# Performance work log

Measured on AMD Instinct MI355X. Metric: run time of the kernel, lower is better.

## Reference

```python
import jax, jax.numpy as jnp
import numpy as np

D_MODEL = 1024
NUM_HEADS = 16
D_K = D_MODEL // NUM_HEADS


def setup_inputs() -> dict:
    key = jax.random.key(0)
    ks = jax.random.split(key, 11)
    B, S = 4, 2048
    s = 1.0 / np.sqrt(D_MODEL)
    inp = {
        "q": jax.random.normal(ks[0], (B, S, D_MODEL), jnp.float32),
        "k": jax.random.normal(ks[1], (B, S, D_MODEL), jnp.float32),
        "v": jax.random.normal(ks[2], (B, S, D_MODEL), jnp.float32),
        "w_q": jax.random.normal(ks[3], (D_MODEL, D_MODEL), jnp.float32) * s,
        "b_q": jnp.zeros((D_MODEL,), jnp.float32),
        "w_k": jax.random.normal(ks[4], (D_MODEL, D_MODEL), jnp.float32) * s,
        "b_k": jnp.zeros((D_MODEL,), jnp.float32),
        "w_v": jax.random.normal(ks[5], (D_MODEL, D_MODEL), jnp.float32) * s,
        "b_v": jnp.zeros((D_MODEL,), jnp.float32),
        "w_o": jax.random.normal(ks[6], (D_MODEL, D_MODEL), jnp.float32) * s,
        "b_o": jnp.zeros((D_MODEL,), jnp.float32),
    }
    return inp


def reference(q, k, v, w_q, b_q, w_k, b_k, w_v, b_v, w_o, b_o):
    B, S, _ = q.shape
    # projections; weights stored as [in, out] so x @ W + b
    def proj(x, w, b):
        y = x @ w + b  # [B, S, d_model]
        return y.reshape(B, -1, NUM_HEADS, D_K).transpose(0, 2, 1, 3)  # [B,H,S,d_k]
    qh = proj(q, w_q, b_q)
    kh = proj(k, w_k, b_k)
    vh = proj(v, w_v, b_v)
    scores = jnp.einsum("bhsd,bhtd->bhst", qh, kh) / jnp.sqrt(jnp.float32(D_K))
    attn = jax.nn.softmax(scores, axis=-1)  # dropout p=0.0 -> identity
    x = jnp.einsum("bhst,bhtd->bhsd", attn, vh)
    x = x.transpose(0, 2, 1, 3).reshape(B, S, D_MODEL)
    return x @ w_o + b_o
```

## Files before the change

### kernel.cpp

```cpp
#include <hip/hip_runtime.h>
#include <hip/hip_bf16.h>
#include <stdint.h>

#define D_MODEL 1024
#define SEQ 2048
#define BATCH 4
#define NHEADS 16
#define ROWS (BATCH*SEQ)

#define QKSCALE 0.18033688011f

typedef __attribute__((ext_vector_type(4))) float f32x4;
typedef __attribute__((ext_vector_type(8))) short short8;
typedef __attribute__((ext_vector_type(4))) unsigned int uint4v;

#if __has_builtin(__builtin_amdgcn_exp2f)
#define EXP2(x) __builtin_amdgcn_exp2f(x)
#else
#define EXP2(x) exp2f(x)
#endif

__device__ __forceinline__ unsigned short f2bf(float f) {
    unsigned int x = __builtin_bit_cast(unsigned int, f);
    x += 0x7fffu + ((x >> 16) & 1u);
    return (unsigned short)(x >> 16);
}

__device__ __forceinline__ unsigned int cvtpk(float a, float b) {
    unsigned int r;
    asm("v_cvt_pk_bf16_f32 %0, %1, %2" : "=v"(r) : "v"(a), "v"(b));
    return r;
}

__device__ __forceinline__ void gload16(const unsigned short* src, unsigned short* dst) {
    __builtin_amdgcn_global_load_lds(
        (const __attribute__((address_space(1))) void*)src,
        (__attribute__((address_space(3))) void*)dst, 16, 0, 0);
}

__global__ __launch_bounds__(256) void wtrans_kernel(const float* __restrict__ w0,
                                                     const float* __restrict__ w1,
                                                     const float* __restrict__ w2,
                                                     const float* __restrict__ w3,
                                                     unsigned short* __restrict__ wt0,
                                                     unsigned short* __restrict__ wt1,
                                                     unsigned short* __restrict__ wt2,
                                                     unsigned short* __restrict__ wt3) {
    const int z = blockIdx.z;
    const float* w = (z == 0) ? w0 : (z == 1) ? w1 : (z == 2) ? w2 : w3;
    unsigned short* wt = (z == 0) ? wt0 : (z == 1) ? wt1 : (z == 2) ? wt2 : wt3;
    __shared__ float tile[32][33];
    int tx = threadIdx.x & 31;
    int ty = threadIdx.x >> 5;
    int r0 = blockIdx.y * 32, c0 = blockIdx.x * 32;
    #pragma unroll
    for (int i = 0; i < 4; ++i)
        tile[ty + 8*i][tx] = w[(size_t)(r0 + ty + 8*i) * D_MODEL + (c0 + tx)];
    __syncthreads();
    int t = threadIdx.x;
    if (t < 128) {
        int n_loc = t >> 2;
        int kc = t & 3;
        int n = c0 + n_loc;
        int kbase = r0 + kc*8;
        uint4v pk;
        #pragma unroll
        for (int j = 0; j < 4; ++j)
            pk[j] = cvtpk(tile[kc*8 + 2*j][n_loc], tile[kc*8 + 2*j + 1][n_loc]);
        size_t tidx = (size_t)(n >> 7) * 16 + (kbase >> 6);
        int row = n & 127;
        int byte = (row*128 + (kbase & 63)*2) ^ ((row & 7) << 4);
        *(uint4v*)((char*)wt + tidx*16384 + byte) = pk;
    }
}

__global__ __launch_bounds__(256) void qkv_gemm_kernel(
        const float* __restrict__ qin, const float* __restrict__ kin,
        const float* __restrict__ vin,
        const unsigned short* __restrict__ wqt, const unsigned short* __restrict__ wkt,
        const unsigned short* __restrict__ wvt,
        const float* __restrict__ bq, const float* __restrict__ bk,
        const float* __restrict__ bv,
        unsigned short* __restrict__ qhd, unsigned short* __restrict__ khd,
        unsigned short* __restrict__ vtd) {
    __shared__ __attribute__((aligned(16))) unsigned short Alds[128*64];
    __shared__ __attribute__((aligned(16))) unsigned short Blds[2][128*64];
    const int z = blockIdx.z;
    const float* Af = (z == 0) ? qin : (z == 1) ? kin : vin;
    const unsigned short* Bt = (z == 0) ? wqt : (z == 1) ? wkt : wvt;
    const float* bias = (z == 0) ? bq : (z == 1) ? bk : bv;
    const int m0 = blockIdx.x * 128;
    const int n0 = blockIdx.y * 128;
    const int t = threadIdx.x;
    const int lane = t & 63;
    const int w = t >> 6;
    const int wm = w >> 1, wn = w & 1;
    const int l15 = lane & 15, lg = lane >> 4;
    const unsigned short* tbase = Bt + (size_t)(n0 >> 7) * 16 * 8192;

    f32x4 acc[4][4];
    #pragma unroll
    for (int i = 0; i < 4; ++i)
        #pragma unroll
        for (int j = 0; j < 4; ++j) acc[i][j] = (f32x4)(0.0f);

    #pragma unroll
    for (int i = 0; i < 8; ++i) {
        int idx = t + i*256;
        int row = idx >> 4, c4 = idx & 15;
        f32x4 v = *(const f32x4*)(Af + (size_t)(m0+row)*D_MODEL + c4*4);
        unsigned long long pk = (unsigned long long)cvtpk(v[0], v[1])
                              | ((unsigned long long)cvtpk(v[2], v[3]) << 32);
        int byte = (row*128 + c4*8) ^ ((row & 7) << 4);
        *(unsigned long long*)((char*)Alds + byte) = pk;
    }
    #pragma unroll
    for (int i = 0; i < 4; ++i)
        gload16(tbase + t*8 + i*2048, Blds[0] + t*8 + i*2048);
    __syncthreads();

    #pragma unroll 2
    for (int kt = 0; kt < 16; ++kt) {
        const int cur = kt & 1, nxt = cur ^ 1;
        f32x4 av[8];
        if (kt < 15) {
            const int k0n = (kt + 1) * 64;
            #pragma unroll
            for (int i = 0; i < 8; ++i) {
                int idx = t + i*256;
                int row = idx >> 4, c4 = idx & 15;
                av[i] = *(const f32x4*)(Af + (size_t)(m0+row)*D_MODEL + k0n + c4*4);
            }
            const unsigned short* tsrc = tbase + (size_t)(kt + 1) * 8192;
            #pragma unroll
            for (int i = 0; i < 4; ++i)
                gload16(tsrc + t*8 + i*2048, Blds[nxt] + t*8 + i*2048);
        }

        #pragma unroll
        for (int kk = 0; kk < 2; ++kk) {
            short8 af[4], bfr[4];
            #pragma unroll
            for (int mi = 0; mi < 4; ++mi) {
                int row = wm*64 + mi*16 + l15;
                int byte = (row*128 + kk*64 + lg*16) ^ ((row & 7) << 4);
                af[mi] = *(const short8*)((const char*)Alds + byte);
            }
            #pragma unroll
            for (int ni = 0; ni < 4; ++ni) {
                int row = wn*64 + ni*16 + l15;
                int byte = (row*128 + kk*64 + lg*16) ^ ((row & 7) << 4);
                bfr[ni] = *(const short8*)((const char*)Blds[cur] + byte);
            }
            #pragma unroll
            for (int mi = 0; mi < 4; ++mi)
                #pragma unroll
                for (int ni = 0; ni < 4; ++ni)
                    acc[mi][ni] = __builtin_amdgcn_mfma_f32_16x16x32_bf16(
                        af[mi], bfr[ni], acc[mi][ni], 0, 0, 0);
        }
        __syncthreads();
        if (kt < 15) {
            #pragma unroll
            for (int i = 0; i < 8; ++i) {
                int idx = t + i*256;
                int row = idx >> 4, c4 = idx & 15;
                unsigned long long pk = (unsigned long long)cvtpk(av[i][0], av[i][1])
                                      | ((unsigned long long)cvtpk(av[i][2], av[i][3]) << 32);
                int byte = (row*128 + c4*8) ^ ((row & 7) << 4);
                *(unsigned long long*)((char*)Alds + byte) = pk;
            }
            __syncthreads();
        }
    }

    #pragma unroll
    for (int mi = 0; mi < 4; ++mi)
        #pragma unroll
        for (int ni = 0; ni < 4; ++ni) {
            int col = n0 + wn*64 + ni*16 + l15;
            float bv_ = bias[col];
            int h = col >> 6, d = col & 63;
            if (z == 0) {
                #pragma unroll
                for (int r = 0; r < 4; ++r) {
                    int row = m0 + wm*64 + mi*16 + lg*4 + r;
                    int bb = row >> 11, s = row & 2047;
                    float vv = (acc[mi][ni][r] + bv_) * QKSCALE;
                    qhd[(((size_t)(bb*NHEADS + h)*SEQ + s) << 6) + d] = f2bf(vv);
                }
            } else if (z == 1) {
                #pragma unroll
                for (int r = 0; r < 4; ++r) {
                    int row = m0 + wm*64 + mi*16 + lg*4 + r;
                    int bb = row >> 11, s = row & 2047;
                    int ti = s >> 6, kvl = s & 63;
                    int ph = (kvl & 0x23) | ((kvl & 4) << 2) | ((kvl & 0x18) >> 1);
                    int byte = (ph*128 + d*2) ^ ((ph & 7) << 4);
                    *(unsigned short*)((char*)khd
                        + ((size_t)(bb*NHEADS + h)*32 + ti)*8192 + byte)
                        = f2bf(acc[mi][ni][r] + bv_);
                }
            } else {
                int row0 = m0 + wm*64 + mi*16 + lg*4;
                int bb = row0 >> 11, s0 = row0 & 2047;
                int ti = s0 >> 6, kvl0 = s0 & 63;
                unsigned long long pk = 0;
                #pragma unroll
                for (int r = 0; r < 4; ++r)
                    pk |= (unsigned long long)f2bf(acc[mi][ni][r] + bv_) << (16*r);
                int byte = (d*128 + kvl0*2) ^ ((d & 7) << 4);
                *(unsigned long long*)((char*)vtd
                    + ((size_t)(bb*NHEADS + h)*32 + ti)*8192 + byte) = pk;
            }
        }
}

__global__ __launch_bounds__(256) void out_gemm_kernel(const unsigned short* __restrict__ Ab,
                                                       const unsigned short* __restrict__ Bt,
                                                       const float* __restrict__ bias,
                                                       float* __restrict__ Out) {
    __shared__ __attribute__((aligned(16))) unsigned short Alds[128*64];
    __shared__ __attribute__((aligned(16))) unsigned short Blds[2][128*64];
    const int m0 = blockIdx.x * 128;
    const int n0 = blockIdx.y * 128;
    const int t = threadIdx.x;
    const int lane = t & 63;
    const int w = t >> 6;
    const int wm = w >> 1, wn = w & 1;
    const int l15 = lane & 15, lg = lane >> 4;
    const unsigned short* tbase = Bt + (size_t)(n0 >> 7) * 16 * 8192;

    f32x4 acc[4][4];
    #pragma unroll
    for (int i = 0; i < 4; ++i)
        #pragma unroll
        for (int j = 0; j < 4; ++j) acc[i][j] = (f32x4)(0.0f);

    #pragma unroll
    for (int i = 0; i < 4; ++i) {
        int idx = t + i*256;
        int row = idx >> 3, c8 = idx & 7;
        short8 v = *(const short8*)(Ab + (size_t)(m0+row)*D_MODEL + c8*8);
        int byte = (row*128 + c8*16) ^ ((row & 7) << 4);
        *(short8*)((char*)Alds + byte) = v;
    }
    #pragma unroll
    for (int i = 0; i < 4; ++i)
        gload16(tbase + t*8 + i*2048, Blds[0] + t*8 + i*2048);
    __syncthreads();

    #pragma unroll 2
    for (int kt = 0; kt < 16; ++kt) {
        const int cur = kt & 1, nxt = cur ^ 1;
        short8 av8[4];
        if (kt < 15) {
            const int k0n = (kt + 1) * 64;
            #pragma unroll
            for (int i = 0; i < 4; ++i) {
                int idx = t + i*256;
                int row = idx >> 3, c8 = idx & 7;
                av8[i] = *(const short8*)(Ab + (size_t)(m0+row)*D_MODEL + k0n + c8*8);
            }
            const unsigned short* tsrc = tbase + (size_t)(kt + 1) * 8192;
            #pragma unroll
            for (int i = 0; i < 4; ++i)
                gload16(tsrc + t*8 + i*2048, Blds[nxt] + t*8 + i*2048);
        }

        #pragma unroll
        for (int kk = 0; kk < 2; ++kk) {
            short8 af[4], bfr[4];
            #pragma unroll
            for (int mi = 0; mi < 4; ++mi) {
                int row = wm*64 + mi*16 + l15;
                int byte = (row*128 + kk*64 + lg*16) ^ ((row & 7) << 4);
                af[mi] = *(const short8*)((const char*)Alds + byte);
            }
            #pragma unroll
            for (int ni = 0; ni < 4; ++ni) {
                int row = wn*64 + ni*16 + l15;
                int byte = (row*128 + kk*64 + lg*16) ^ ((row & 7) << 4);
                bfr[ni] = *(const short8*)((const char*)Blds[cur] + byte);
            }
            #pragma unroll
            for (int mi = 0; mi < 4; ++mi)
                #pragma unroll
                for (int ni = 0; ni < 4; ++ni)
                    acc[mi][ni] = __builtin_amdgcn_mfma_f32_16x16x32_bf16(
                        af[mi], bfr[ni], acc[mi][ni], 0, 0, 0);
        }
        __syncthreads();
        if (kt < 15) {
            #pragma unroll
            for (int i = 0; i < 4; ++i) {
                int idx = t + i*256;
                int row = idx >> 3, c8 = idx & 7;
                int byte = (row*128 + c8*16) ^ ((row & 7) << 4);
                *(short8*)((char*)Alds + byte) = av8[i];
            }
            __syncthreads();
        }
    }

    #pragma unroll
    for (int mi = 0; mi < 4; ++mi)
        #pragma unroll
        for (int ni = 0; ni < 4; ++ni) {
            int col = n0 + wn*64 + ni*16 + l15;
            float bv_ = bias[col];
            #pragma unroll
            for (int r = 0; r < 4; ++r) {
                int row = m0 + wm*64 + mi*16 + lg*4 + r;
                Out[(size_t)row*D_MODEL + col] = acc[mi][ni][r] + bv_;
            }
        }
}

__global__ __launch_bounds__(256, 4) void attn_kernel(const unsigned short* __restrict__ qh,
                                                      const unsigned short* __restrict__ kimg_all,
                                                      const unsigned short* __restrict__ vimg_all,
                                                      unsigned short* __restrict__ xout) {
    __shared__ __attribute__((aligned(16))) unsigned short Klds[2][64*64];
    __shared__ __attribute__((aligned(16))) unsigned short Vtl[2][64*64];

    const int bid = blockIdx.x;
    const int xcd = bid & 7, idx = bid >> 3;
    const int qb = idx >> 3;
    const int bh = ((idx & 7) << 3) | xcd;
    const int t = threadIdx.x;
    const int lane = t & 63;
    const int w = t >> 6;
    const int l15 = lane & 15, lg = lane >> 4;

    const unsigned short* qbase = qh + (size_t)bh * SEQ * 64;
    const unsigned short* kimg = kimg_all + (size_t)bh * SEQ * 64;
    const unsigned short* vimg = vimg_all + (size_t)bh * SEQ * 64;

    short8 qf[2][2];
    #pragma unroll
    for (int l = 0; l < 2; ++l) {
        int qrow = qb*128 + w*32 + l*16 + l15;
        qf[l][0] = *(const short8*)(qbase + (size_t)qrow*64 + lg*8);
        qf[l][1] = *(const short8*)(qbase + (size_t)qrow*64 + 32 + lg*8);
    }

    int fb[4][2];
    #pragma unroll
    for (int nb = 0; nb < 4; ++nb) {
        int rr = nb*16 + l15;
        int sw = (rr & 7) << 4;
        fb[nb][0] = (rr*128 + lg*16) ^ sw;
        fb[nb][1] = (rr*128 + 64 + lg*16) ^ sw;
    }

    float m[2] = {-1e30f, -1e30f};
    float lsum[2] = {0.f, 0.f};
    f32x4 o[2][4];
    #pragma unroll
    for (int l = 0; l < 2; ++l)
        #pragma unroll
        for (int nb = 0; nb < 4; ++nb) o[l][nb] = (f32x4)(0.0f);

    #pragma unroll
    for (int i = 0; i < 2; ++i) {
        __builtin_amdgcn_global_load_lds(
            (const __attribute__((address_space(1))) void*)(kimg + t*8 + i*2048),
            (__attribute__((address_space(3))) void*)(Klds[0] + t*8 + i*2048), 16, 0, 0);
        __builtin_amdgcn_global_load_lds(
            (const __attribute__((address_space(1))) void*)(vimg + t*8 + i*2048),
            (__attribute__((address_space(3))) void*)(Vtl[0] + t*8 + i*2048), 16, 0, 0);
    }
    __syncthreads();

    const unsigned short* kp = kimg + 4096 + t*8;
    const unsigned short* vp = vimg + 4096 + t*8;

    const int NT = SEQ/64;
    #pragma unroll 2
    for (int ti = 0; ti < NT; ++ti) {
        const int c = ti & 1;
        if (ti + 1 < NT) {
            #pragma unroll
            for (int i = 0; i < 2; ++i) {
                __builtin_amdgcn_global_load_lds(
                    (const __attribute__((address_space(1))) void*)(kp + i*2048),
                    (__attribute__((address_space(3))) void*)(Klds[c^1] + t*8 + i*2048), 16, 0, 0);
                __builtin_amdgcn_global_load_lds(
                    (const __attribute__((address_space(1))) void*)(vp + i*2048),
                    (__attribute__((address_space(3))) void*)(Vtl[c^1] + t*8 + i*2048), 16, 0, 0);
            }
            kp += 4096; vp += 4096;
        }
        const char* Kc = (const char*)Klds[c];
        const char* Vc = (const char*)Vtl[c];

        f32x4 s4[2][4];
        #pragma unroll
        for (int nb = 0; nb < 4; ++nb) {
            short8 kf0 = *(const short8*)(Kc + fb[nb][0]);
            short8 kf1 = *(const short8*)(Kc + fb[nb][1]);
            __builtin_amdgcn_s_setprio(1);
            #pragma unroll
            for (int l = 0; l < 2; ++l) {
                f32x4 s = (f32x4)(0.0f);
                s = __builtin_amdgcn_mfma_f32_16x16x32_bf16(kf0, qf[l][0], s, 0, 0, 0);
                s = __builtin_amdgcn_mfma_f32_16x16x32_bf16(kf1, qf[l][1], s, 0, 0, 0);
                s4[l][nb] = s;
            }
            __builtin_amdgcn_s_setprio(0);
        }

        if (ti == 0) {
            #pragma unroll
            for (int l = 0; l < 2; ++l) {
                float tm = s4[l][0][0];
                #pragma unroll
                for (int nb = 0; nb < 4; ++nb)
                    #pragma unroll
                    for (int r = 0; r < 4; ++r) tm = fmaxf(tm, s4[l][nb][r]);
                tm = fmaxf(tm, __shfl_xor(tm, 16));
                tm = fmaxf(tm, __shfl_xor(tm, 32));
                m[l] = tm;
            }
        }

        union U { short8 s; unsigned int u[4]; } pa[2][2];
        #pragma unroll
        for (int l = 0; l < 2; ++l) {
            float p[16];
            float ts = 0.f;
            #pragma unroll
            for (int nb = 0; nb < 4; ++nb)
                #pragma unroll
                for (int r = 0; r < 4; ++r) {
                    float pv = EXP2(s4[l][nb][r] - m[l]);
                    p[nb*4 + r] = pv;
                    ts += pv;
                }
            lsum[l] += ts;

            pa[l][0].u[0] = cvtpk(p[0],  p[1]);  pa[l][0].u[1] = cvtpk(p[2],  p[3]);
            pa[l][0].u[2] = cvtpk(p[4],  p[5]);  pa[l][0].u[3] = cvtpk(p[6],  p[7]);
            pa[l][1].u[0] = cvtpk(p[8],  p[9]);  pa[l][1].u[1] = cvtpk(p[10], p[11]);
            pa[l][1].u[2] = cvtpk(p[12], p[13]); pa[l][1].u[3] = cvtpk(p[14], p[15]);
        }

        #pragma unroll
        for (int nb = 0; nb < 4; ++nb) {
            short8 vf0 = *(const short8*)(Vc + fb[nb][0]);
            short8 vf1 = *(const short8*)(Vc + fb[nb][1]);
            __builtin_amdgcn_s_setprio(1);
            o[0][nb] = __builtin_amdgcn_mfma_f32_16x16x32_bf16(pa[0][0].s, vf0, o[0][nb], 0, 0, 0);
            o[0][nb] = __builtin_amdgcn_mfma_f32_16x16x32_bf16(pa[0][1].s, vf1, o[0][nb], 0, 0, 0);
            o[1][nb] = __builtin_amdgcn_mfma_f32_16x16x32_bf16(pa[1][0].s, vf0, o[1][nb], 0, 0, 0);
            o[1][nb] = __builtin_amdgcn_mfma_f32_16x16x32_bf16(pa[1][1].s, vf1, o[1][nb], 0, 0, 0);
            __builtin_amdgcn_s_setprio(0);
        }

        __syncthreads();
    }

    const int bb = bh >> 4, h = bh & 15;
    #pragma unroll
    for (int l = 0; l < 2; ++l) {
        float lt = lsum[l];
        lt += __shfl_xor(lt, 16);
        lt += __shfl_xor(lt, 32);
        float rl[4];
        #pragma unroll
        for (int r = 0; r < 4; ++r) rl[r] = 1.0f / __shfl(lt, lg*4 + r);
        #pragma unroll
        for (int nb = 0; nb < 4; ++nb)
            #pragma unroll
            for (int r = 0; r < 4; ++r) {
                int s = qb*128 + w*32 + l*16 + lg*4 + r;
                int d = nb*16 + l15;
                xout[((size_t)(bb*SEQ + s))*D_MODEL + h*64 + d] = f2bf(o[l][nb][r] * rl[r]);
            }
    }
}

extern "C" void kernel_launch(void* const* d_in, const int* in_sizes, int n_in,
                              void* d_out, int out_size, void* d_ws, size_t ws_size,
                              hipStream_t stream) {
    (void)in_sizes; (void)n_in; (void)out_size; (void)ws_size;
    const float* q  = (const float*)d_in[0];
    const float* k  = (const float*)d_in[1];
    const float* v  = (const float*)d_in[2];
    const float* wq = (const float*)d_in[3];
    const float* bq = (const float*)d_in[4];
    const float* wk = (const float*)d_in[5];
    const float* bk = (const float*)d_in[6];
    const float* wv = (const float*)d_in[7];
    const float* bv = (const float*)d_in[8];
    const float* wo = (const float*)d_in[9];
    const float* bo = (const float*)d_in[10];

    char* ws = (char*)d_ws;
    unsigned short* wqt = (unsigned short*)(ws);
    unsigned short* wkt = (unsigned short*)(ws + (2ull << 20));
    unsigned short* wvt = (unsigned short*)(ws + (4ull << 20));
    unsigned short* wot = (unsigned short*)(ws + (6ull << 20));
    unsigned short* qhd = (unsigned short*)(ws + (8ull << 20));
    unsigned short* khd = (unsigned short*)(ws + (24ull << 20));
    unsigned short* vtd = (unsigned short*)(ws + (40ull << 20));
    unsigned short* xat = (unsigned short*)(ws + (56ull << 20));

    hipLaunchKernelGGL(wtrans_kernel, dim3(D_MODEL/32, D_MODEL/32, 4), dim3(256), 0, stream,
                       wq, wk, wv, wo, wqt, wkt, wvt, wot);

    hipLaunchKernelGGL(qkv_gemm_kernel, dim3(ROWS/128, D_MODEL/128, 3), dim3(256), 0, stream,
                       q, k, v, wqt, wkt, wvt, bq, bk, bv, qhd, khd, vtd);

    hipLaunchKernelGGL(attn_kernel, dim3(16*64), dim3(256), 0, stream,
                       qhd, khd, vtd, xat);

    hipLaunchKernelGGL(out_gemm_kernel, dim3(ROWS/128, D_MODEL/128), dim3(256), 0, stream,
                       xat, wot, bo, (float*)d_out);
}
```

Baseline: 189.4 us.

## Software-pipeline attention loop: overlap QK^T of next tile with PV of previous

Restructures the attention inner loop so each iteration computes QK^T for tile ti while doing the PV matmul for tile ti-1 with already-packed probabilities, then runs softmax on the new scores. V is triple-buffered in LDS to keep the previous tile alive while prefetching. The aim is to hide exp/softmax latency behind MFMA work. It adds a prologue and epilogue and uses more LDS, which may reduce occupancy. The loop is also no longer unrolled.

```diff
diff --git a/kernel.cpp b/kernel.cpp
--- a/kernel.cpp
+++ b/kernel.cpp
@@ -322,7 +322,7 @@
                                                       const unsigned short* __restrict__ vimg_all,
                                                       unsigned short* __restrict__ xout) {
     __shared__ __attribute__((aligned(16))) unsigned short Klds[2][64*64];
-    __shared__ __attribute__((aligned(16))) unsigned short Vtl[2][64*64];
+    __shared__ __attribute__((aligned(16))) unsigned short Vtl[3][64*64];
 
     const int bid = blockIdx.x;
     const int xcd = bid & 7, idx = bid >> 3;
@@ -362,70 +362,10 @@
         #pragma unroll
         for (int nb = 0; nb < 4; ++nb) o[l][nb] = (f32x4)(0.0f);
 
-    #pragma unroll
-    for (int i = 0; i < 2; ++i) {
-        __builtin_amdgcn_global_load_lds(
-            (const __attribute__((address_space(1))) void*)(kimg + t*8 + i*2048),
-            (__attribute__((address_space(3))) void*)(Klds[0] + t*8 + i*2048), 16, 0, 0);
-        __builtin_amdgcn_global_load_lds(
-            (const __attribute__((address_space(1))) void*)(vimg + t*8 + i*2048),
-            (__attribute__((address_space(3))) void*)(Vtl[0] + t*8 + i*2048), 16, 0, 0);
-    }
-    __syncthreads();
-
-    const unsigned short* kp = kimg + 4096 + t*8;
-    const unsigned short* vp = vimg + 4096 + t*8;
-
-    const int NT = SEQ/64;
-    #pragma unroll 2
-    for (int ti = 0; ti < NT; ++ti) {
-        const int c = ti & 1;
-        if (ti + 1 < NT) {
-            #pragma unroll
-            for (int i = 0; i < 2; ++i) {
-                __builtin_amdgcn_global_load_lds(
-                    (const __attribute__((address_space(1))) void*)(kp + i*2048),
-                    (__attribute__((address_space(3))) void*)(Klds[c^1] + t*8 + i*2048), 16, 0, 0);
-                __builtin_amdgcn_global_load_lds(
-                    (const __attribute__((address_space(1))) void*)(vp + i*2048),
-                    (__attribute__((address_space(3))) void*)(Vtl[c^1] + t*8 + i*2048), 16, 0, 0);
-            }
-            kp += 4096; vp += 4096;
-        }
-        const char* Kc = (const char*)Klds[c];
-        const char* Vc = (const char*)Vtl[c];
-
-        f32x4 s4[2][4];
-        #pragma unroll
-        for (int nb = 0; nb < 4; ++nb) {
-            short8 kf0 = *(const short8*)(Kc + fb[nb][0]);
-            short8 kf1 = *(const short8*)(Kc + fb[nb][1]);
-            __builtin_amdgcn_s_setprio(1);
-            #pragma unroll
-            for (int l = 0; l < 2; ++l) {
-                f32x4 s = (f32x4)(0.0f);
-                s = __builtin_amdgcn_mfma_f32_16x16x32_bf16(kf0, qf[l][0], s, 0, 0, 0);
-                s = __builtin_amdgcn_mfma_f32_16x16x32_bf16(kf1, qf[l][1], s, 0, 0, 0);
-                s4[l][nb] = s;
-            }
-            __builtin_amdgcn_s_setprio(0);
-        }
-
-        if (ti == 0) {
-            #pragma unroll
-            for (int l = 0; l < 2; ++l) {
-                float tm = s4[l][0][0];
-                #pragma unroll
-                for (int nb = 0; nb < 4; ++nb)
-                    #pragma unroll
-                    for (int r = 0; r < 4; ++r) tm = fmaxf(tm, s4[l][nb][r]);
-                tm = fmaxf(tm, __shfl_xor(tm, 16));
-                tm = fmaxf(tm, __shfl_xor(tm, 32));
-                m[l] = tm;
-            }
-        }
-
-        union U { short8 s; unsigned int u[4]; } pa[2][2];
+    union U { short8 s; unsigned int u[4]; };
+    U pa[2][2];
+
+    auto softmax_pack = [&](f32x4 s4[2][4]) {
         #pragma unroll
         for (int l = 0; l < 2; ++l) {
             float p[16];
@@ -439,17 +379,95 @@
                     ts += pv;
                 }
             lsum[l] += ts;
-
             pa[l][0].u[0] = cvtpk(p[0],  p[1]);  pa[l][0].u[1] = cvtpk(p[2],  p[3]);
             pa[l][0].u[2] = cvtpk(p[4],  p[5]);  pa[l][0].u[3] = cvtpk(p[6],  p[7]);
             pa[l][1].u[0] = cvtpk(p[8],  p[9]);  pa[l][1].u[1] = cvtpk(p[10], p[11]);
             pa[l][1].u[2] = cvtpk(p[12], p[13]); pa[l][1].u[3] = cvtpk(p[14], p[15]);
         }
-
+    };
+
+    #pragma unroll
+    for (int i = 0; i < 2; ++i) {
+        gload16(kimg + t*8 + i*2048, Klds[0] + t*8 + i*2048);
+        gload16(vimg + t*8 + i*2048, Vtl[0] + t*8 + i*2048);
+    }
+    __syncthreads();
+
+    const int NT = SEQ/64;
+
+    {
+        #pragma unroll
+        for (int i = 0; i < 2; ++i) {
+            gload16(kimg + 4096 + t*8 + i*2048, Klds[1] + t*8 + i*2048);
+            gload16(vimg + 4096 + t*8 + i*2048, Vtl[1] + t*8 + i*2048);
+        }
+        f32x4 s4[2][4];
         #pragma unroll
         for (int nb = 0; nb < 4; ++nb) {
-            short8 vf0 = *(const short8*)(Vc + fb[nb][0]);
-            short8 vf1 = *(const short8*)(Vc + fb[nb][1]);
+            short8 kf0 = *(const short8*)((const char*)Klds[0] + fb[nb][0]);
+            short8 kf1 = *(const short8*)((const char*)Klds[0] + fb[nb][1]);
+            __builtin_amdgcn_s_setprio(1);
+            #pragma unroll
+            for (int l = 0; l < 2; ++l) {
+                f32x4 s = (f32x4)(0.0f);
+                s = __builtin_amdgcn_mfma_f32_16x16x32_bf16(kf0, qf[l][0], s, 0, 0, 0);
+                s = __builtin_amdgcn_mfma_f32_16x16x32_bf16(kf1, qf[l][1], s, 0, 0, 0);
+                s4[l][nb] = s;
+            }
+            __builtin_amdgcn_s_setprio(0);
+        }
+        #pragma unroll
+        for (int l = 0; l < 2; ++l) {
+            float tm = s4[l][0][0];
+            #pragma unroll
+            for (int nb = 0; nb < 4; ++nb)
+                #pragma unroll
+                for (int r = 0; r < 4; ++r) tm = fmaxf(tm, s4[l][nb][r]);
+            tm = fmaxf(tm, __shfl_xor(tm, 16));
+            tm = fmaxf(tm, __shfl_xor(tm, 32));
+            m[l] = tm;
+        }
+        softmax_pack(s4);
+        __syncthreads();
+    }
+
+    int kc_ = 1;
+    int vprev = 0;
+    int vw = 2;
+    #pragma unroll 1
+    for (int ti = 1; ti < NT; ++ti) {
+        if (ti + 1 < NT) {
+            const unsigned short* ks = kimg + (size_t)(ti + 1)*4096 + t*8;
+            const unsigned short* vs = vimg + (size_t)(ti + 1)*4096 + t*8;
+            #pragma unroll
+            for (int i = 0; i < 2; ++i) {
+                gload16(ks + i*2048, Klds[kc_^1] + t*8 + i*2048);
+                gload16(vs + i*2048, Vtl[vw] + t*8 + i*2048);
+            }
+        }
+        const char* Kc = (const char*)Klds[kc_];
+        const char* Vp = (const char*)Vtl[vprev];
+
+        f32x4 s4[2][4];
+        #pragma unroll
+        for (int nb = 0; nb < 4; ++nb) {
+            short8 kf0 = *(const short8*)(Kc + fb[nb][0]);
+            short8 kf1 = *(const short8*)(Kc + fb[nb][1]);
+            __builtin_amdgcn_s_setprio(1);
+            #pragma unroll
+            for (int l = 0; l < 2; ++l) {
+                f32x4 s = (f32x4)(0.0f);
+                s = __builtin_amdgcn_mfma_f32_16x16x32_bf16(kf0, qf[l][0], s, 0, 0, 0);
+                s = __builtin_amdgcn_mfma_f32_16x16x32_bf16(kf1, qf[l][1], s, 0, 0, 0);
+                s4[l][nb] = s;
+            }
+            __builtin_amdgcn_s_setprio(0);
+        }
+
+        #pragma unroll
+        for (int nb = 0; nb < 4; ++nb) {
+            short8 vf0 = *(const short8*)(Vp + fb[nb][0]);
+            short8 vf1 = *(const short8*)(Vp + fb[nb][1]);
             __builtin_amdgcn_s_setprio(1);
             o[0][nb] = __builtin_amdgcn_mfma_f32_16x16x32_bf16(pa[0][0].s, vf0, o[0][nb], 0, 0, 0);
             o[0][nb] = __builtin_amdgcn_mfma_f32_16x16x32_bf16(pa[0][1].s, vf1, o[0][nb], 0, 0, 0);
@@ -458,7 +476,25 @@
             __builtin_amdgcn_s_setprio(0);
         }
 
+        softmax_pack(s4);
+
         __syncthreads();
+        kc_ ^= 1;
+        vprev = (vprev == 2) ? 0 : vprev + 1;
+        vw    = (vw == 2)    ? 0 : vw + 1;
+    }
+
+    {
+        const char* Vp = (const char*)Vtl[vprev];
+        #pragma unroll
+        for (int nb = 0; nb < 4; ++nb) {
+            short8 vf0 = *(const short8*)(Vp + fb[nb][0]);
+            short8 vf1 = *(const short8*)(Vp + fb[nb][1]);
+            o[0][nb] = __builtin_amdgcn_mfma_f32_16x16x32_bf16(pa[0][0].s, vf0, o[0][nb], 0, 0, 0);
+            o[0][nb] = __builtin_amdgcn_mfma_f32_16x16x32_bf16(pa[0][1].s, vf1, o[0][nb], 0, 0, 0);
+            o[1][nb] = __builtin_amdgcn_mfma_f32_16x16x32_bf16(pa[1][0].s, vf0, o[1][nb], 0, 0, 0);
+            o[1][nb] = __builtin_amdgcn_mfma_f32_16x16x32_bf16(pa[1][1].s, vf1, o[1][nb], 0, 0, 0);
+        }
     }
 
     const int bb = bh >> 4, h = bh & 15;
```

Result: no change. 190.8 us (+0.7%).
